# Performance work log

Hardware: AMD Instinct MI355X
Metric: run time of the kernel (lower is better)

Reference implementation:

```python
import jax, jax.numpy as jnp
import numpy as np

B, N, DN = 8, 4096, 64
E = 1048576
H, DM = 128, 64   # message MLP: 2*DN -> H -> DM
HU, F = 128, 64   # node-update MLP: DN+DM -> HU -> F


def setup_inputs() -> dict:
    key = jax.random.key(0)
    ks = jax.random.split(key, 13)
    inp = {
        'node_feats': jax.random.normal(ks[0], (B, N, DN), dtype=jnp.float32),
        'edge_b': jax.random.randint(ks[1], (E,), 0, B, dtype=jnp.int32),
        'edge_src': jax.random.randint(ks[2], (E,), 0, N, dtype=jnp.int32),
        'edge_dst': jax.random.randint(ks[3], (E,), 0, N, dtype=jnp.int32),
        'edge_vals': jax.random.uniform(ks[4], (E,), dtype=jnp.float32),
        # message MLP params (Dense-relu, Dense-linear)
        'Wm1': jax.random.normal(ks[5], (2 * DN, H), dtype=jnp.float32) / np.sqrt(2 * DN),
        'bm1': jnp.zeros((H,), jnp.float32),
        'Wm2': jax.random.normal(ks[6], (H, DM), dtype=jnp.float32) / np.sqrt(H),
        'bm2': jnp.zeros((DM,), jnp.float32),
        # node-update MLP params
        'Wu1': jax.random.normal(ks[7], (DN + DM, HU), dtype=jnp.float32) / np.sqrt(DN + DM),
        'bu1': jnp.zeros((HU,), jnp.float32),
        'Wu2': jax.random.normal(ks[8], (HU, F), dtype=jnp.float32) / np.sqrt(HU),
        'bu2': jnp.zeros((F,), jnp.float32),
    }
    return inp


def reference(node_feats, edge_b, edge_src, edge_dst, edge_vals,
              Wm1, bm1, Wm2, bm2, Wu1, bu1, Wu2, bu2):
    # --- create messages: gather src/target feats per edge ---
    src_feats = node_feats[edge_b, edge_src]            # (E, DN)
    tgt_feats = node_feats[edge_b, edge_dst]            # (E, DN)
    feats = jnp.concatenate([src_feats, tgt_feats], axis=-1)  # (E, 2*DN)
    h = jax.nn.relu(feats @ Wm1 + bm1)
    messages = h @ Wm2 + bm2                            # (E, DM)

    # --- gather (scatter) messages: weighted ragged segment-mean ---
    weighted = messages * edge_vals[:, None]            # (E, DM)
    seg = edge_b * N + edge_src                          # rowids b*max_N + src
    sums = jax.ops.segment_sum(weighted, seg, num_segments=B * N)
    counts = jax.ops.segment_sum(jnp.ones((E,), weighted.dtype), seg,
                                 num_segments=B * N)
    gathered = sums / jnp.maximum(counts, 1.0)[:, None]  # mean; 0 for empty rows
    gathered = gathered.reshape(B, N, DM)

    # --- update nodes ---
    upd_in = jnp.concatenate([node_feats, gathered], axis=-1)  # (B, N, DN+DM)
    hu = jax.nn.relu(upd_in @ Wu1 + bu1)
    updated = hu @ Wu2 + bu2                            # (B, N, F)
    return updated
```

## Files before the change

### kernel.cpp

```cpp
#include <hip/hip_runtime.h>

#define NB 8
#define NN 4096
#define DNF 64
#define NEDGE 1048576
#define DM 64
#define FF 64

#define NBKT2 2048
#define SPB2 16
#define NXCD 8
#define SUBCAP 176
#define OVFCAP 32768
#define SCATBLK 2048

using f32x4 = __attribute__((ext_vector_type(4))) float;
using f32x2 = __attribute__((ext_vector_type(2))) float;
using s16x8 = __attribute__((ext_vector_type(8))) short;

__device__ __forceinline__ unsigned short f2b(float f) {
    union { float f; unsigned u; } v; v.f = f;
    unsigned r = (v.u + 0x7fffu + ((v.u >> 16) & 1u)) >> 16;
    return (unsigned short)r;
}
__device__ __forceinline__ float uif(unsigned u) {
    union { unsigned u; float f; } v; v.u = u;
    return v.f;
}

__device__ __forceinline__ void pack_one(const float* __restrict__ W,
                                         unsigned short* __restrict__ out,
                                         int K, int Ncols, int idx) {
    int j = idx & 7;
    int lane = (idx >> 3) & 63;
    int frag = idx >> 9;
    int KS = K >> 5;
    int ks = frag % KS;
    int nt = frag / KS;
    int k = ks * 32 + ((lane >> 4) << 3) + j;
    int col = nt * 16 + (lane & 15);
    out[idx] = f2b(W[k * Ncols + col]);
}

__global__ void pack_all(const float* __restrict__ Wm1, const float* __restrict__ Wm2,
                         const float* __restrict__ Wu1, const float* __restrict__ Wu2,
                         unsigned short* __restrict__ Qw, unsigned short* __restrict__ Pw,
                         unsigned short* __restrict__ Wm2p,
                         unsigned short* __restrict__ Wu1p, unsigned short* __restrict__ Wu2p) {
    int idx = blockIdx.x * 256 + threadIdx.x;
    if (idx < 8192)        pack_one(Wm1,              Qw,   64, 128, idx);
    else if (idx < 16384)  pack_one(Wm1 + 64 * 128,   Pw,   64, 128, idx - 8192);
    else if (idx < 24576)  pack_one(Wm2,              Wm2p, 128, 64, idx - 16384);
    else if (idx < 40960)  pack_one(Wu1,              Wu1p, 128, 128, idx - 24576);
    else                   pack_one(Wu2,              Wu2p, 128, 64, idx - 40960);
}

__global__ void pack_weights(const float* __restrict__ W, unsigned short* __restrict__ out,
                             int K, int Ncols) {
    int idx = blockIdx.x * 256 + threadIdx.x;
    if (idx >= K * Ncols) return;
    pack_one(W, out, K, Ncols, idx);
}

__launch_bounds__(256, 6)
__global__ void scatter_pq(const int* __restrict__ eb, const int* __restrict__ esrc,
                           const int* __restrict__ edst, const float* __restrict__ evals,
                           unsigned* __restrict__ gcurP, unsigned* __restrict__ payslot,
                           unsigned* __restrict__ ovf_cnt, unsigned* __restrict__ ovf_seg,
                           unsigned* __restrict__ ovf_pay,
                           const float* __restrict__ X,
                           const unsigned short* __restrict__ Qw,
                           const unsigned short* __restrict__ Pw,
                           const float* __restrict__ b1,
                           unsigned short* __restrict__ Qp,
                           unsigned short* __restrict__ Pp) {
    __shared__ unsigned short A[64][72];
    if (blockIdx.x < SCATBLK) {
        unsigned xcd;
        asm volatile("s_getreg_b32 %0, hwreg(HW_REG_XCC_ID)" : "=s"(xcd));
        xcd &= (NXCD - 1);
        const int t0 = blockIdx.x * 512 + threadIdx.x;
        int seg[2]; unsigned pk[2];
#pragma unroll
        for (int k = 0; k < 2; ++k) {
            int e = t0 + k * 256;
            seg[k] = eb[e] * NN + esrc[e];
            unsigned wq = (unsigned)fminf(evals[e] * 8192.0f + 0.5f, 8191.0f);
            pk[k] = (unsigned)edst[e] | (wq << 12) | ((unsigned)(seg[k] & 15) << 25);
        }
        unsigned pos[2];
#pragma unroll
        for (int k = 0; k < 2; ++k)
            pos[k] = atomicAdd(&gcurP[((int)xcd * NBKT2 + (seg[k] >> 4)) * 16], 1u);
#pragma unroll
        for (int k = 0; k < 2; ++k) {
            if (pos[k] < (unsigned)SUBCAP) {
                payslot[((size_t)(seg[k] >> 4) * NXCD + xcd) * SUBCAP + pos[k]] = pk[k];
            } else {
                unsigned o = atomicAdd(ovf_cnt, 1u);
                if (o < (unsigned)OVFCAP) { ovf_seg[o] = (unsigned)seg[k]; ovf_pay[o] = pk[k]; }
            }
        }
    } else {
        const int tid = threadIdx.x;
        const int g0 = (blockIdx.x - SCATBLK) * 64;
        for (int i = 0; i < 16; ++i) {
            int idx = i * 256 + tid;
            int node = idx >> 6;
            int f = idx & 63;
            A[node][f] = f2b(X[(size_t)(g0 + node) * DNF + f]);
        }
        __syncthreads();
        const int wave = tid >> 6, lane = tid & 63;
        const int lr = lane & 15, lq = lane >> 4;
        const int arow = wave * 16 + lr;
        s16x8 a[2];
#pragma unroll
        for (int ks = 0; ks < 2; ++ks)
            a[ks] = *reinterpret_cast<const s16x8*>(&A[arow][ks * 32 + lq * 8]);
#pragma unroll
        for (int nt = 0; nt < 8; ++nt) {
            f32x4 accQ = {0.f, 0.f, 0.f, 0.f};
            f32x4 accP = {0.f, 0.f, 0.f, 0.f};
#pragma unroll
            for (int ks = 0; ks < 2; ++ks) {
                s16x8 bq = *reinterpret_cast<const s16x8*>(&Qw[(((nt << 1) + ks) * 64 + lane) * 8]);
                s16x8 bp = *reinterpret_cast<const s16x8*>(&Pw[(((nt << 1) + ks) * 64 + lane) * 8]);
                accQ = __builtin_amdgcn_mfma_f32_16x16x32_bf16(a[ks], bq, accQ, 0, 0, 0);
                accP = __builtin_amdgcn_mfma_f32_16x16x32_bf16(a[ks], bp, accP, 0, 0, 0);
            }
            int col = nt * 16 + lr;
            float bias = b1[col];
#pragma unroll
            for (int j = 0; j < 4; ++j) {
                int row = g0 + wave * 16 + lq * 4 + j;
                Qp[(size_t)row * 128 + col] = f2b(accQ[j] + bias);
                Pp[(size_t)row * 128 + col] = f2b(accP[j]);
            }
        }
    }
}

__launch_bounds__(256, 6)
__global__ void bucket16_fused(const unsigned short* __restrict__ Qp,
                               const unsigned short* __restrict__ Pp,
                               const unsigned* __restrict__ payslot,
                               const unsigned* __restrict__ gcurP,
                               const unsigned* __restrict__ ovf_cnt,
                               const unsigned* __restrict__ ovf_seg,
                               const unsigned* __restrict__ ovf_pay,
                               const unsigned short* __restrict__ Wm2p,
                               const float* __restrict__ b2m,
                               const float* __restrict__ X,
                               const unsigned short* __restrict__ Wu1p,
                               const float* __restrict__ bu1,
                               const unsigned short* __restrict__ Wu2p,
                               const float* __restrict__ bu2,
                               float* __restrict__ out) {
    __shared__ unsigned raw[NXCD * SUBCAP];
    __shared__ unsigned sorted[NXCD * SUBCAP];
    __shared__ unsigned short S[16][136];
    __shared__ unsigned short A1[16][136];
    __shared__ unsigned short Hs[16][136];
    __shared__ unsigned h4[4][16];
    __shared__ unsigned curb4[4][16];
    __shared__ unsigned offs[17];
    __shared__ unsigned cx[NXCD];
    __shared__ float SW[16], SC[16];
    const int tid = threadIdx.x, wv = tid >> 6, lane = tid & 63;
    const int bkt = (blockIdx.x & 7) * 256 + (blockIdx.x >> 3);
    const int node0 = bkt * SPB2;
    const int rowbase = (bkt >> 8) << 12;
    const unsigned novf = ovf_cnt[0];

#pragma unroll
    for (int i = 0; i < 4; ++i) {
        int idx = i * 256 + tid;
        int row = idx >> 6, f = idx & 63;
        A1[row][f] = f2b(X[(size_t)(node0 + row) * DNF + f]);
    }
    if (tid < 64) ((unsigned*)h4)[tid] = 0;
    if (tid < NXCD) cx[tid] = min(gcurP[(tid * NBKT2 + bkt) * 16], (unsigned)SUBCAP);
    __syncthreads();
#pragma unroll
    for (int xi = 0; xi < 2; ++xi) {
        int x = wv * 2 + xi;
        unsigned c = cx[x];
        for (unsigned i = lane; i < c; i += 64) {
            unsigned v = payslot[((size_t)bkt * NXCD + x) * SUBCAP + i];
            raw[x * SUBCAP + i] = v;
            atomicAdd(&h4[wv][(v >> 25) & 15u], 1u);
        }
    }
    __syncthreads();
    if (tid < 16) {
        int xx = (int)(h4[0][tid] + h4[1][tid] + h4[2][tid] + h4[3][tid]);
#pragma unroll
        for (int o = 1; o < 16; o <<= 1) {
            int y = __shfl_up(xx, o);
            if (tid >= o) xx += y;
        }
        offs[tid + 1] = (unsigned)xx;
        if (tid == 0) offs[0] = 0;
    }
    __syncthreads();
    if (tid < 64) {
        int w = tid >> 4, b = tid & 15;
        unsigned base = offs[b];
        for (int w2 = 0; w2 < w; ++w2) base += h4[w2][b];
        curb4[w][b] = base;
    }
    __syncthreads();
#pragma unroll
    for (int xi = 0; xi < 2; ++xi) {
        int x = wv * 2 + xi;
        unsigned c = cx[x];
        for (unsigned i = lane; i < c; i += 64) {
            unsigned v = raw[x * SUBCAP + i];
            unsigned pos = atomicAdd(&curb4[wv][(v >> 25) & 15u], 1u);
            sorted[pos] = v;
        }
    }
    __syncthreads();

    const unsigned* P32 = reinterpret_cast<const unsigned*>(Pp);
    const unsigned* Q32 = reinterpret_cast<const unsigned*>(Qp);
    const unsigned* PbS = P32 + (size_t)rowbase * 64;
    for (int si = 0; si < 4; ++si) {
        const int lo = wv * 4 + si;
        const int seg = node0 + lo;
        const unsigned s0 = offs[lo], s1 = offs[lo + 1];
        unsigned qv = Q32[(size_t)seg * 64 + lane];
        f32x2 q2 = { uif(qv << 16), uif(qv & 0xffff0000u) };
        f32x2 acc2 = { 0.f, 0.f };
        unsigned scnt = s1 - s0;

        float wl = 0.f;
        for (unsigned i = s0 + lane; i < s1; i += 64)
            wl += (float)((sorted[i] >> 12) & 8191u);
        for (int m2 = 1; m2 < 64; m2 <<= 1) wl += __shfl_xor(wl, m2);
        float wsum = wl;

        for (unsigned bse = s0; bse < s1; bse += 8) {
            unsigned pv[8]; float wf[8];
#pragma unroll
            for (int k = 0; k < 8; ++k) {
                unsigned idx = bse + (unsigned)k;
                unsigned cu = (idx < s1) ? sorted[idx] : 0u;
                int ci = __builtin_amdgcn_readfirstlane((int)cu);
                wf[k] = (float)(unsigned)((ci >> 12) & 8191);
                int row = ci & 0xfff;
                pv[k] = PbS[(size_t)row * 64 + lane];
            }
#pragma unroll
            for (int k = 0; k < 8; ++k) {
                f32x2 p2 = { uif(pv[k] << 16), uif(pv[k] & 0xffff0000u) };
                f32x2 h2 = q2 + p2;
                h2 = __builtin_elementwise_max(h2, (f32x2){0.f, 0.f});
                acc2 += wf[k] * h2;
            }
        }
        if (novf > 0) {
            unsigned ncl = min(novf, (unsigned)OVFCAP);
            for (unsigned i = 0; i < ncl; ++i) {
                if (ovf_seg[i] == (unsigned)seg) {
                    unsigned c = ovf_pay[i];
                    float w = (float)((c >> 12) & 8191u);
                    unsigned pv = PbS[(size_t)(c & 0xfffu) * 64 + lane];
                    f32x2 p2 = { uif(pv << 16), uif(pv & 0xffff0000u) };
                    f32x2 h2 = q2 + p2;
                    h2 = __builtin_elementwise_max(h2, (f32x2){0.f, 0.f});
                    acc2 += w * h2;
                    wsum += w;
                    scnt += 1;
                }
            }
        }
        unsigned sp = (unsigned)f2b(acc2.x) | ((unsigned)f2b(acc2.y) << 16);
        *reinterpret_cast<unsigned*>(&S[lo][2 * lane]) = sp;
        if (lane == 0) {
            SW[lo] = wsum;
            SC[lo] = (1.0f / 8192.0f) / (float)max(scnt, 1u);
        }
    }
    __syncthreads();

    const int lr = lane & 15, lq = lane >> 4;
    {
        s16x8 a[4];
#pragma unroll
        for (int ks = 0; ks < 4; ++ks)
            a[ks] = *reinterpret_cast<const s16x8*>(&S[lr][ks * 32 + lq * 8]);
        f32x4 acc = {0.f, 0.f, 0.f, 0.f};
#pragma unroll
        for (int ks = 0; ks < 4; ++ks) {
            s16x8 bf = *reinterpret_cast<const s16x8*>(&Wm2p[(((wv << 2) + ks) * 64 + lane) * 8]);
            acc = __builtin_amdgcn_mfma_f32_16x16x32_bf16(a[ks], bf, acc, 0, 0, 0);
        }
        float bb = b2m[wv * 16 + lr];
#pragma unroll
        for (int j = 0; j < 4; ++j) {
            int r = lq * 4 + j;
            float g = (acc[j] + SW[r] * bb) * SC[r];
            A1[r][64 + wv * 16 + lr] = f2b(g);
        }
    }
    __syncthreads();

    {
        s16x8 a1[4];
#pragma unroll
        for (int ks = 0; ks < 4; ++ks)
            a1[ks] = *reinterpret_cast<const s16x8*>(&A1[lr][ks * 32 + lq * 8]);
#pragma unroll
        for (int t = 0; t < 2; ++t) {
            int nt = wv * 2 + t;
            f32x4 acc = {0.f, 0.f, 0.f, 0.f};
#pragma unroll
            for (int ks = 0; ks < 4; ++ks) {
                s16x8 bf = *reinterpret_cast<const s16x8*>(&Wu1p[(((nt << 2) + ks) * 64 + lane) * 8]);
                acc = __builtin_amdgcn_mfma_f32_16x16x32_bf16(a1[ks], bf, acc, 0, 0, 0);
            }
            float bias = bu1[nt * 16 + lr];
#pragma unroll
            for (int j = 0; j < 4; ++j) {
                float hh = fmaxf(acc[j] + bias, 0.f);
                Hs[lq * 4 + j][nt * 16 + lr] = f2b(hh);
            }
        }
    }
    __syncthreads();

    {
        s16x8 a2[4];
#pragma unroll
        for (int ks = 0; ks < 4; ++ks)
            a2[ks] = *reinterpret_cast<const s16x8*>(&Hs[lr][ks * 32 + lq * 8]);
        f32x4 acc = {0.f, 0.f, 0.f, 0.f};
#pragma unroll
        for (int ks = 0; ks < 4; ++ks) {
            s16x8 bf = *reinterpret_cast<const s16x8*>(&Wu2p[(((wv << 2) + ks) * 64 + lane) * 8]);
            acc = __builtin_amdgcn_mfma_f32_16x16x32_bf16(a2[ks], bf, acc, 0, 0, 0);
        }
        float bias = bu2[wv * 16 + lr];
#pragma unroll
        for (int j = 0; j < 4; ++j)
            out[(size_t)(node0 + lq * 4 + j) * FF + wv * 16 + lr] = acc[j] + bias;
    }
}


template<int SCALE>
__launch_bounds__(256, 4)
__global__ void node_kernel(const float* __restrict__ node_feats,
                            const float* __restrict__ sums, const float* __restrict__ counts,
                            const unsigned short* __restrict__ W1p, const float* __restrict__ b1,
                            const unsigned short* __restrict__ W2p, const float* __restrict__ b2,
                            float* __restrict__ out) {
    __shared__ unsigned short A1[64][136];
    __shared__ unsigned short Hs[64][136];
    const int tid = threadIdx.x;
    const int g0 = blockIdx.x * 64;
    for (int i = 0; i < 16; ++i) {
        int idx = i * 256 + tid;
        int node = idx >> 6;
        int p = idx & 63;
        int g = g0 + node;
        float2 v;
        if (p < 32) {
            v = *reinterpret_cast<const float2*>(node_feats + (size_t)g * DNF + 2 * p);
        } else {
            float2 s = *reinterpret_cast<const float2*>(sums + (size_t)g * DM + 2 * p - 64);
            if (SCALE) {
                float scale = 1.0f / fmaxf(counts[g], 1.0f);
                s.x *= scale; s.y *= scale;
            }
            v = s;
        }
        unsigned packed = (unsigned)f2b(v.x) | ((unsigned)f2b(v.y) << 16);
        *reinterpret_cast<unsigned*>(&A1[node][2 * p]) = packed;
    }
    __syncthreads();
    const int wave = tid >> 6, lane = tid & 63;
    const int lr = lane & 15, lq = lane >> 4;
    const int arow = wave * 16 + lr;
    s16x8 a[4];
#pragma unroll
    for (int ks = 0; ks < 4; ++ks)
        a[ks] = *reinterpret_cast<const s16x8*>(&A1[arow][ks * 32 + lq * 8]);
#pragma unroll
    for (int nt = 0; nt < 8; ++nt) {
        f32x4 acc = {0.f, 0.f, 0.f, 0.f};
#pragma unroll
        for (int ks = 0; ks < 4; ++ks) {
            s16x8 bf = *reinterpret_cast<const s16x8*>(&W1p[(((nt << 2) + ks) * 64 + lane) * 8]);
            acc = __builtin_amdgcn_mfma_f32_16x16x32_bf16(a[ks], bf, acc, 0, 0, 0);
        }
        float bias = b1[nt * 16 + lr];
#pragma unroll
        for (int j = 0; j < 4; ++j) {
            float h = acc[j] + bias;
            h = h > 0.f ? h : 0.f;
            Hs[wave * 16 + lq * 4 + j][nt * 16 + lr] = f2b(h);
        }
    }
    s16x8 a2[4];
#pragma unroll
    for (int ks = 0; ks < 4; ++ks)
        a2[ks] = *reinterpret_cast<const s16x8*>(&Hs[arow][ks * 32 + lq * 8]);
#pragma unroll
    for (int nt = 0; nt < 4; ++nt) {
        f32x4 acc = {0.f, 0.f, 0.f, 0.f};
#pragma unroll
        for (int ks = 0; ks < 4; ++ks) {
            s16x8 bf = *reinterpret_cast<const s16x8*>(&W2p[(((nt << 2) + ks) * 64 + lane) * 8]);
            acc = __builtin_amdgcn_mfma_f32_16x16x32_bf16(a2[ks], bf, acc, 0, 0, 0);
        }
        float bias = b2[nt * 16 + lr];
#pragma unroll
        for (int j = 0; j < 4; ++j) {
            int g = g0 + wave * 16 + lq * 4 + j;
            out[(size_t)g * FF + nt * 16 + lr] = acc[j] + bias;
        }
    }
}

__launch_bounds__(256, 4)
__global__ void edge_kernel(const float* __restrict__ node_feats,
                            const int* __restrict__ eb, const int* __restrict__ esrc,
                            const int* __restrict__ edst, const float* __restrict__ evals,
                            const unsigned short* __restrict__ W1p, const float* __restrict__ b1,
                            const unsigned short* __restrict__ W2p, const float* __restrict__ b2,
                            float* __restrict__ sums, float* __restrict__ counts) {
    __shared__ unsigned short A1[64][136];
    __shared__ unsigned short Hs[64][136];
    const int tid = threadIdx.x;
    const int e0 = blockIdx.x * 64;
    if (tid < 64) {
        int e = e0 + tid;
        atomicAdd(&counts[eb[e] * NN + esrc[e]], 1.0f);
    }
    for (int i = 0; i < 16; ++i) {
        int idx = i * 256 + tid;
        int edge = idx >> 6;
        int p = idx & 63;
        int e = e0 + edge;
        int b = eb[e];
        const float* row;
        if (p < 32) row = node_feats + ((size_t)b * NN + esrc[e]) * DNF;
        else        row = node_feats + ((size_t)b * NN + edst[e]) * DNF - 64;
        float2 v = *reinterpret_cast<const float2*>(row + 2 * p);
        unsigned packed = (unsigned)f2b(v.x) | ((unsigned)f2b(v.y) << 16);
        *reinterpret_cast<unsigned*>(&A1[edge][2 * p]) = packed;
    }
    __syncthreads();
    const int wave = tid >> 6, lane = tid & 63;
    const int lr = lane & 15, lq = lane >> 4;
    const int arow = wave * 16 + lr;
    s16x8 a[4];
#pragma unroll
    for (int ks = 0; ks < 4; ++ks)
        a[ks] = *reinterpret_cast<const s16x8*>(&A1[arow][ks * 32 + lq * 8]);
#pragma unroll
    for (int nt = 0; nt < 8; ++nt) {
        f32x4 acc = {0.f, 0.f, 0.f, 0.f};
#pragma unroll
        for (int ks = 0; ks < 4; ++ks) {
            s16x8 bf = *reinterpret_cast<const s16x8*>(&W1p[(((nt << 2) + ks) * 64 + lane) * 8]);
            acc = __builtin_amdgcn_mfma_f32_16x16x32_bf16(a[ks], bf, acc, 0, 0, 0);
        }
        float bias = b1[nt * 16 + lr];
#pragma unroll
        for (int j = 0; j < 4; ++j) {
            float h = acc[j] + bias;
            h = h > 0.f ? h : 0.f;
            Hs[wave * 16 + lq * 4 + j][nt * 16 + lr] = f2b(h);
        }
    }
    s16x8 a2[4];
#pragma unroll
    for (int ks = 0; ks < 4; ++ks)
        a2[ks] = *reinterpret_cast<const s16x8*>(&Hs[arow][ks * 32 + lq * 8]);
    float ev[4]; int seg4[4];
#pragma unroll
    for (int j = 0; j < 4; ++j) {
        int r = e0 + wave * 16 + lq * 4 + j;
        ev[j] = evals[r];
        seg4[j] = eb[r] * NN + esrc[r];
    }
#pragma unroll
    for (int nt = 0; nt < 4; ++nt) {
        f32x4 acc = {0.f, 0.f, 0.f, 0.f};
#pragma unroll
        for (int ks = 0; ks < 4; ++ks) {
            s16x8 bf = *reinterpret_cast<const s16x8*>(&W2p[(((nt << 2) + ks) * 64 + lane) * 8]);
            acc = __builtin_amdgcn_mfma_f32_16x16x32_bf16(a2[ks], bf, acc, 0, 0, 0);
        }
        float bias = b2[nt * 16 + lr];
#pragma unroll
        for (int j = 0; j < 4; ++j) {
            float m = (acc[j] + bias) * ev[j];
            atomicAdd(&sums[(size_t)seg4[j] * DM + nt * 16 + lr], m);
        }
    }
}

extern "C" void kernel_launch(void* const* d_in, const int* in_sizes, int n_in,
                              void* d_out, int out_size, void* d_ws, size_t ws_size,
                              hipStream_t stream) {
    const float* node_feats = (const float*)d_in[0];
    const int*   eb    = (const int*)d_in[1];
    const int*   esrc  = (const int*)d_in[2];
    const int*   edst  = (const int*)d_in[3];
    const float* evals = (const float*)d_in[4];
    const float* Wm1 = (const float*)d_in[5];
    const float* bm1 = (const float*)d_in[6];
    const float* Wm2 = (const float*)d_in[7];
    const float* bm2 = (const float*)d_in[8];
    const float* Wu1 = (const float*)d_in[9];
    const float* bu1 = (const float*)d_in[10];
    const float* Wu2 = (const float*)d_in[11];
    const float* bu2 = (const float*)d_in[12];
    float* out = (float*)d_out;
    char* ws = (char*)d_ws;

    const size_t NEED = 29720704;
    if (ws_size >= NEED) {
        unsigned short* Qp      = (unsigned short*)(ws);
        unsigned short* Pp      = (unsigned short*)(ws + 8388608);
        unsigned*       payslot = (unsigned*)(ws + 16777216);
        unsigned*       gcurP   = (unsigned*)(ws + 28311552);
        unsigned*       ovf_cnt = (unsigned*)(ws + 29360128);
        unsigned*       ovf_seg = (unsigned*)(ws + 29360256);
        unsigned*       ovf_pay = (unsigned*)(ws + 29491328);
        unsigned short* Qw      = (unsigned short*)(ws + 29622400);
        unsigned short* Pw      = (unsigned short*)(ws + 29638784);
        unsigned short* Wu1p    = (unsigned short*)(ws + 29655168);
        unsigned short* Wu2p    = (unsigned short*)(ws + 29687936);
        unsigned short* Wm2p    = (unsigned short*)(ws + 29704320);

        hipMemsetAsync(gcurP, 0, 1048576 + 128, stream);
        pack_all<<<192, 256, 0, stream>>>(Wm1, Wm2, Wu1, Wu2, Qw, Pw, Wm2p, Wu1p, Wu2p);
        scatter_pq<<<SCATBLK + 512, 256, 0, stream>>>(eb, esrc, edst, evals,
                                                      gcurP, payslot, ovf_cnt, ovf_seg, ovf_pay,
                                                      node_feats, Qw, Pw, bm1, Qp, Pp);
        bucket16_fused<<<NBKT2, 256, 0, stream>>>(Qp, Pp, payslot, gcurP,
                                                  ovf_cnt, ovf_seg, ovf_pay,
                                                  Wm2p, bm2, node_feats,
                                                  Wu1p, bu1, Wu2p, bu2, out);
    } else {
        float* counts          = (float*)ws;
        unsigned short* W1p    = (unsigned short*)(ws + 131072);
        unsigned short* W2p    = (unsigned short*)(ws + 163840);
        unsigned short* Wu1p   = (unsigned short*)(ws + 180224);
        unsigned short* Wu2p   = (unsigned short*)(ws + 212992);
        hipMemsetAsync(d_out, 0, (size_t)out_size * sizeof(float), stream);
        hipMemsetAsync(counts, 0, 32768 * sizeof(float), stream);
        pack_weights<<<64, 256, 0, stream>>>(Wm1, W1p, 128, 128);
        pack_weights<<<32, 256, 0, stream>>>(Wm2, W2p, 128, 64);
        pack_weights<<<64, 256, 0, stream>>>(Wu1, Wu1p, 128, 128);
        pack_weights<<<32, 256, 0, stream>>>(Wu2, Wu2p, 128, 64);
        edge_kernel<<<NEDGE / 64, 256, 0, stream>>>(node_feats, eb, esrc, edst, evals,
                                                    W1p, bm1, W2p, bm2, out, counts);
        node_kernel<1><<<(NB * NN) / 64, 256, 0, stream>>>(node_feats, out, counts,
                                                           Wu1p, bu1, Wu2p, bu2, out);
    }
}
```

Baseline: 111.3 us.

## Replace atomic bucket scatter with histogram-scan counting sort of edges

Edges are now bucketed by a two-pass counting sort: per-block LDS histograms, a column-wise and total prefix scan, then a scatter using LDS atomic cursors into contiguous bucket ranges. The consumer kernel walks each bucket's exact range in chunks instead of fixed-capacity per-XCD slots plus an overflow list. This removes contended global atomics, the memset and the overflow scan. In exchange it adds extra kernel launches, a second read of edge indices, and a serial column scan with low parallelism.

After: 101.9 us. -8.4%, faster.

```diff
diff --git a/kernel.cpp b/kernel.cpp
--- a/kernel.cpp
+++ b/kernel.cpp
@@ -9,10 +9,9 @@
 
 #define NBKT2 2048
 #define SPB2 16
-#define NXCD 8
-#define SUBCAP 176
-#define OVFCAP 32768
-#define SCATBLK 2048
+#define SORTBLK 512
+#define EPB 2048
+#define CHUNK 1024
 
 using f32x4 = __attribute__((ext_vector_type(4))) float;
 using f32x2 = __attribute__((ext_vector_type(2))) float;
@@ -62,48 +61,33 @@
     pack_one(W, out, K, Ncols, idx);
 }
 
-__launch_bounds__(256, 6)
-__global__ void scatter_pq(const int* __restrict__ eb, const int* __restrict__ esrc,
-                           const int* __restrict__ edst, const float* __restrict__ evals,
-                           unsigned* __restrict__ gcurP, unsigned* __restrict__ payslot,
-                           unsigned* __restrict__ ovf_cnt, unsigned* __restrict__ ovf_seg,
-                           unsigned* __restrict__ ovf_pay,
-                           const float* __restrict__ X,
-                           const unsigned short* __restrict__ Qw,
-                           const unsigned short* __restrict__ Pw,
-                           const float* __restrict__ b1,
-                           unsigned short* __restrict__ Qp,
-                           unsigned short* __restrict__ Pp) {
-    __shared__ unsigned short A[64][72];
-    if (blockIdx.x < SCATBLK) {
-        unsigned xcd;
-        asm volatile("s_getreg_b32 %0, hwreg(HW_REG_XCC_ID)" : "=s"(xcd));
-        xcd &= (NXCD - 1);
-        const int t0 = blockIdx.x * 512 + threadIdx.x;
-        int seg[2]; unsigned pk[2];
-#pragma unroll
-        for (int k = 0; k < 2; ++k) {
-            int e = t0 + k * 256;
-            seg[k] = eb[e] * NN + esrc[e];
-            unsigned wq = (unsigned)fminf(evals[e] * 8192.0f + 0.5f, 8191.0f);
-            pk[k] = (unsigned)edst[e] | (wq << 12) | ((unsigned)(seg[k] & 15) << 25);
-        }
-        unsigned pos[2];
-#pragma unroll
-        for (int k = 0; k < 2; ++k)
-            pos[k] = atomicAdd(&gcurP[((int)xcd * NBKT2 + (seg[k] >> 4)) * 16], 1u);
-#pragma unroll
-        for (int k = 0; k < 2; ++k) {
-            if (pos[k] < (unsigned)SUBCAP) {
-                payslot[((size_t)(seg[k] >> 4) * NXCD + xcd) * SUBCAP + pos[k]] = pk[k];
-            } else {
-                unsigned o = atomicAdd(ovf_cnt, 1u);
-                if (o < (unsigned)OVFCAP) { ovf_seg[o] = (unsigned)seg[k]; ovf_pay[o] = pk[k]; }
-            }
-        }
+__launch_bounds__(256, 8)
+__global__ void hist_pq(const int* __restrict__ eb, const int* __restrict__ esrc,
+                        unsigned* __restrict__ histm,
+                        const float* __restrict__ X,
+                        const unsigned short* __restrict__ Qw,
+                        const unsigned short* __restrict__ Pw,
+                        const float* __restrict__ b1,
+                        unsigned short* __restrict__ Qp,
+                        unsigned short* __restrict__ Pp) {
+    __shared__ unsigned lds_u[2304];
+    const int tid = threadIdx.x;
+    if (blockIdx.x < SORTBLK) {
+        unsigned* bins = lds_u;
+        for (int i = tid; i < NBKT2; i += 256) bins[i] = 0;
+        __syncthreads();
+        const int e0 = blockIdx.x * EPB;
+#pragma unroll
+        for (int i = 0; i < EPB / 256; ++i) {
+            int e = e0 + i * 256 + tid;
+            atomicAdd(&bins[(eb[e] * NN + esrc[e]) >> 4], 1u);
+        }
+        __syncthreads();
+        for (int i = tid; i < NBKT2; i += 256)
+            histm[(size_t)blockIdx.x * NBKT2 + i] = bins[i];
     } else {
-        const int tid = threadIdx.x;
-        const int g0 = (blockIdx.x - SCATBLK) * 64;
+        unsigned short (*A)[72] = reinterpret_cast<unsigned short(*)[72]>(lds_u);
+        const int g0 = (blockIdx.x - SORTBLK) * 64;
         for (int i = 0; i < 16; ++i) {
             int idx = i * 256 + tid;
             int node = idx >> 6;
@@ -141,14 +125,67 @@
     }
 }
 
+__launch_bounds__(256)
+__global__ void scan_cols(unsigned* __restrict__ histm, unsigned* __restrict__ total) {
+    const int col = blockIdx.x * 256 + threadIdx.x;
+    unsigned run = 0;
+    for (int b = 0; b < SORTBLK; ++b) {
+        unsigned v = histm[(size_t)b * NBKT2 + col];
+        histm[(size_t)b * NBKT2 + col] = run;
+        run += v;
+    }
+    total[col] = run;
+}
+
+__launch_bounds__(256)
+__global__ void scan_tot(const unsigned* __restrict__ total, unsigned* __restrict__ base) {
+    __shared__ unsigned part[256];
+    const int t = threadIdx.x;
+    unsigned v[8]; unsigned s = 0;
+#pragma unroll
+    for (int i = 0; i < 8; ++i) { v[i] = total[t * 8 + i]; s += v[i]; }
+    part[t] = s;
+    __syncthreads();
+    for (int off = 1; off < 256; off <<= 1) {
+        unsigned x = (t >= off) ? part[t - off] : 0u;
+        __syncthreads();
+        part[t] += x;
+        __syncthreads();
+    }
+    unsigned run = t ? part[t - 1] : 0u;
+#pragma unroll
+    for (int i = 0; i < 8; ++i) { base[t * 8 + i] = run; run += v[i]; }
+    if (t == 255) base[NBKT2] = run;
+}
+
+__launch_bounds__(256, 8)
+__global__ void sort_scatter(const int* __restrict__ eb, const int* __restrict__ esrc,
+                             const int* __restrict__ edst, const float* __restrict__ evals,
+                             const unsigned* __restrict__ histm,
+                             const unsigned* __restrict__ base,
+                             unsigned* __restrict__ payslot) {
+    __shared__ unsigned cur[NBKT2];
+    const int blk = blockIdx.x, tid = threadIdx.x;
+    for (int i = tid; i < NBKT2; i += 256)
+        cur[i] = base[i] + histm[(size_t)blk * NBKT2 + i];
+    __syncthreads();
+    const int e0 = blk * EPB;
+#pragma unroll
+    for (int i = 0; i < EPB / 256; ++i) {
+        int e = e0 + i * 256 + tid;
+        int seg = eb[e] * NN + esrc[e];
+        unsigned wq = (unsigned)fminf(evals[e] * 8192.0f + 0.5f, 8191.0f);
+        unsigned pay = (unsigned)edst[e] | (wq << 12) | ((unsigned)(seg & 15) << 25);
+        unsigned pos = atomicAdd(&cur[seg >> 4], 1u);
+        payslot[pos] = pay;
+    }
+}
+
 __launch_bounds__(256, 6)
 __global__ void bucket16_fused(const unsigned short* __restrict__ Qp,
                                const unsigned short* __restrict__ Pp,
                                const unsigned* __restrict__ payslot,
-                               const unsigned* __restrict__ gcurP,
-                               const unsigned* __restrict__ ovf_cnt,
-                               const unsigned* __restrict__ ovf_seg,
-                               const unsigned* __restrict__ ovf_pay,
+                               const unsigned* __restrict__ gBase,
                                const unsigned short* __restrict__ Wm2p,
                                const float* __restrict__ b2m,
                                const float* __restrict__ X,
@@ -157,21 +194,19 @@
                                const unsigned short* __restrict__ Wu2p,
                                const float* __restrict__ bu2,
                                float* __restrict__ out) {
-    __shared__ unsigned raw[NXCD * SUBCAP];
-    __shared__ unsigned sorted[NXCD * SUBCAP];
+    __shared__ unsigned raw[CHUNK];
+    __shared__ unsigned sorted[CHUNK];
     __shared__ unsigned short S[16][136];
     __shared__ unsigned short A1[16][136];
     __shared__ unsigned short Hs[16][136];
     __shared__ unsigned h4[4][16];
     __shared__ unsigned curb4[4][16];
     __shared__ unsigned offs[17];
-    __shared__ unsigned cx[NXCD];
     __shared__ float SW[16], SC[16];
     const int tid = threadIdx.x, wv = tid >> 6, lane = tid & 63;
     const int bkt = (blockIdx.x & 7) * 256 + (blockIdx.x >> 3);
     const int node0 = bkt * SPB2;
     const int rowbase = (bkt >> 8) << 12;
-    const unsigned novf = ovf_cnt[0];
 
 #pragma unroll
     for (int i = 0; i < 4; ++i) {
@@ -179,108 +214,101 @@
         int row = idx >> 6, f = idx & 63;
         A1[row][f] = f2b(X[(size_t)(node0 + row) * DNF + f]);
     }
-    if (tid < 64) ((unsigned*)h4)[tid] = 0;
-    if (tid < NXCD) cx[tid] = min(gcurP[(tid * NBKT2 + bkt) * 16], (unsigned)SUBCAP);
-    __syncthreads();
-#pragma unroll
-    for (int xi = 0; xi < 2; ++xi) {
-        int x = wv * 2 + xi;
-        unsigned c = cx[x];
-        for (unsigned i = lane; i < c; i += 64) {
-            unsigned v = payslot[((size_t)bkt * NXCD + x) * SUBCAP + i];
-            raw[x * SUBCAP + i] = v;
-            atomicAdd(&h4[wv][(v >> 25) & 15u], 1u);
-        }
-    }
-    __syncthreads();
-    if (tid < 16) {
-        int xx = (int)(h4[0][tid] + h4[1][tid] + h4[2][tid] + h4[3][tid]);
-#pragma unroll
-        for (int o = 1; o < 16; o <<= 1) {
-            int y = __shfl_up(xx, o);
-            if (tid >= o) xx += y;
-        }
-        offs[tid + 1] = (unsigned)xx;
-        if (tid == 0) offs[0] = 0;
-    }
-    __syncthreads();
-    if (tid < 64) {
-        int w = tid >> 4, b = tid & 15;
-        unsigned base = offs[b];
-        for (int w2 = 0; w2 < w; ++w2) base += h4[w2][b];
-        curb4[w][b] = base;
-    }
-    __syncthreads();
-#pragma unroll
-    for (int xi = 0; xi < 2; ++xi) {
-        int x = wv * 2 + xi;
-        unsigned c = cx[x];
-        for (unsigned i = lane; i < c; i += 64) {
-            unsigned v = raw[x * SUBCAP + i];
-            unsigned pos = atomicAdd(&curb4[wv][(v >> 25) & 15u], 1u);
-            sorted[pos] = v;
-        }
-    }
-    __syncthreads();
 
     const unsigned* P32 = reinterpret_cast<const unsigned*>(Pp);
     const unsigned* Q32 = reinterpret_cast<const unsigned*>(Qp);
     const unsigned* PbS = P32 + (size_t)rowbase * 64;
+
+    f32x2 q2[4], acc2[4];
+    float wsum[4];
+    unsigned scnt[4];
+#pragma unroll
+    for (int si = 0; si < 4; ++si) {
+        int lo = wv * 4 + si;
+        unsigned qv = Q32[(size_t)(node0 + lo) * 64 + lane];
+        q2[si].x = uif(qv << 16); q2[si].y = uif(qv & 0xffff0000u);
+        acc2[si].x = 0.f; acc2[si].y = 0.f;
+        wsum[si] = 0.f; scnt[si] = 0u;
+    }
+
+    const unsigned start = gBase[bkt], end = gBase[bkt + 1];
+    for (unsigned cbase = start; cbase < end; cbase += CHUNK) {
+        const unsigned n = min((unsigned)CHUNK, end - cbase);
+        if (tid < 64) ((unsigned*)h4)[tid] = 0;
+        __syncthreads();
+        for (unsigned i = tid; i < n; i += 256) {
+            unsigned v = payslot[cbase + i];
+            raw[i] = v;
+            atomicAdd(&h4[wv][(v >> 25) & 15u], 1u);
+        }
+        __syncthreads();
+        if (tid < 16) {
+            int xx = (int)(h4[0][tid] + h4[1][tid] + h4[2][tid] + h4[3][tid]);
+#pragma unroll
+            for (int o = 1; o < 16; o <<= 1) {
+                int y = __shfl_up(xx, o);
+                if (tid >= o) xx += y;
+            }
+            offs[tid + 1] = (unsigned)xx;
+            if (tid == 0) offs[0] = 0;
+        }
+        __syncthreads();
+        if (tid < 64) {
+            int w = tid >> 4, b = tid & 15;
+            unsigned bse = offs[b];
+            for (int w2 = 0; w2 < w; ++w2) bse += h4[w2][b];
+            curb4[w][b] = bse;
+        }
+        __syncthreads();
+        for (unsigned i = tid; i < n; i += 256) {
+            unsigned v = raw[i];
+            unsigned pos = atomicAdd(&curb4[wv][(v >> 25) & 15u], 1u);
+            sorted[pos] = v;
+        }
+        __syncthreads();
+
+#pragma unroll
+        for (int si = 0; si < 4; ++si) {
+            const int lo = wv * 4 + si;
+            const unsigned s0 = offs[lo], s1 = offs[lo + 1];
+            scnt[si] += s1 - s0;
+            float wl = 0.f;
+            for (unsigned i = s0 + lane; i < s1; i += 64)
+                wl += (float)((sorted[i] >> 12) & 8191u);
+            for (int m2 = 1; m2 < 64; m2 <<= 1) wl += __shfl_xor(wl, m2);
+            wsum[si] += wl;
+
+            for (unsigned bse = s0; bse < s1; bse += 8) {
+                unsigned pv[8]; float wf[8];
+#pragma unroll
+                for (int k = 0; k < 8; ++k) {
+                    unsigned idx = bse + (unsigned)k;
+                    unsigned cu = (idx < s1) ? sorted[idx] : 0u;
+                    int ci = __builtin_amdgcn_readfirstlane((int)cu);
+                    wf[k] = (float)(unsigned)((ci >> 12) & 8191);
+                    int row = ci & 0xfff;
+                    pv[k] = PbS[(size_t)row * 64 + lane];
+                }
+#pragma unroll
+                for (int k = 0; k < 8; ++k) {
+                    f32x2 p2 = { uif(pv[k] << 16), uif(pv[k] & 0xffff0000u) };
+                    f32x2 h2 = q2[si] + p2;
+                    h2 = __builtin_elementwise_max(h2, (f32x2){0.f, 0.f});
+                    acc2[si] += wf[k] * h2;
+                }
+            }
+        }
+        __syncthreads();
+    }
+
+#pragma unroll
     for (int si = 0; si < 4; ++si) {
         const int lo = wv * 4 + si;
-        const int seg = node0 + lo;
-        const unsigned s0 = offs[lo], s1 = offs[lo + 1];
-        unsigned qv = Q32[(size_t)seg * 64 + lane];
-        f32x2 q2 = { uif(qv << 16), uif(qv & 0xffff0000u) };
-        f32x2 acc2 = { 0.f, 0.f };
-        unsigned scnt = s1 - s0;
-
-        float wl = 0.f;
-        for (unsigned i = s0 + lane; i < s1; i += 64)
-            wl += (float)((sorted[i] >> 12) & 8191u);
-        for (int m2 = 1; m2 < 64; m2 <<= 1) wl += __shfl_xor(wl, m2);
-        float wsum = wl;
-
-        for (unsigned bse = s0; bse < s1; bse += 8) {
-            unsigned pv[8]; float wf[8];
-#pragma unroll
-            for (int k = 0; k < 8; ++k) {
-                unsigned idx = bse + (unsigned)k;
-                unsigned cu = (idx < s1) ? sorted[idx] : 0u;
-                int ci = __builtin_amdgcn_readfirstlane((int)cu);
-                wf[k] = (float)(unsigned)((ci >> 12) & 8191);
-                int row = ci & 0xfff;
-                pv[k] = PbS[(size_t)row * 64 + lane];
-            }
-#pragma unroll
-            for (int k = 0; k < 8; ++k) {
-                f32x2 p2 = { uif(pv[k] << 16), uif(pv[k] & 0xffff0000u) };
-                f32x2 h2 = q2 + p2;
-                h2 = __builtin_elementwise_max(h2, (f32x2){0.f, 0.f});
-                acc2 += wf[k] * h2;
-            }
-        }
-        if (novf > 0) {
-            unsigned ncl = min(novf, (unsigned)OVFCAP);
-            for (unsigned i = 0; i < ncl; ++i) {
-                if (ovf_seg[i] == (unsigned)seg) {
-                    unsigned c = ovf_pay[i];
-                    float w = (float)((c >> 12) & 8191u);
-                    unsigned pv = PbS[(size_t)(c & 0xfffu) * 64 + lane];
-                    f32x2 p2 = { uif(pv << 16), uif(pv & 0xffff0000u) };
-                    f32x2 h2 = q2 + p2;
-                    h2 = __builtin_elementwise_max(h2, (f32x2){0.f, 0.f});
-                    acc2 += w * h2;
-                    wsum += w;
-                    scnt += 1;
-                }
-            }
-        }
-        unsigned sp = (unsigned)f2b(acc2.x) | ((unsigned)f2b(acc2.y) << 16);
+        unsigned sp = (unsigned)f2b(acc2[si].x) | ((unsigned)f2b(acc2[si].y) << 16);
         *reinterpret_cast<unsigned*>(&S[lo][2 * lane]) = sp;
         if (lane == 0) {
-            SW[lo] = wsum;
-            SC[lo] = (1.0f / 8192.0f) / (float)max(scnt, 1u);
+            SW[lo] = wsum[si];
+            SC[lo] = (1.0f / 8192.0f) / (float)max(scnt[si], 1u);
         }
     }
     __syncthreads();
@@ -524,28 +552,28 @@
     float* out = (float*)d_out;
     char* ws = (char*)d_ws;
 
-    const size_t NEED = 29720704;
+    const size_t NEED = 25296896;
     if (ws_size >= NEED) {
         unsigned short* Qp      = (unsigned short*)(ws);
         unsigned short* Pp      = (unsigned short*)(ws + 8388608);
         unsigned*       payslot = (unsigned*)(ws + 16777216);
-        unsigned*       gcurP   = (unsigned*)(ws + 28311552);
-        unsigned*       ovf_cnt = (unsigned*)(ws + 29360128);
-        unsigned*       ovf_seg = (unsigned*)(ws + 29360256);
-        unsigned*       ovf_pay = (unsigned*)(ws + 29491328);
-        unsigned short* Qw      = (unsigned short*)(ws + 29622400);
-        unsigned short* Pw      = (unsigned short*)(ws + 29638784);
-        unsigned short* Wu1p    = (unsigned short*)(ws + 29655168);
-        unsigned short* Wu2p    = (unsigned short*)(ws + 29687936);
-        unsigned short* Wm2p    = (unsigned short*)(ws + 29704320);
-
-        hipMemsetAsync(gcurP, 0, 1048576 + 128, stream);
+        unsigned*       histm   = (unsigned*)(ws + 20971520);
+        unsigned*       total   = (unsigned*)(ws + 25165824);
+        unsigned*       bbase   = (unsigned*)(ws + 25182208);
+        unsigned short* Qw      = (unsigned short*)(ws + 25198592);
+        unsigned short* Pw      = (unsigned short*)(ws + 25214976);
+        unsigned short* Wu1p    = (unsigned short*)(ws + 25231360);
+        unsigned short* Wu2p    = (unsigned short*)(ws + 25264128);
+        unsigned short* Wm2p    = (unsigned short*)(ws + 25280512);
+
         pack_all<<<192, 256, 0, stream>>>(Wm1, Wm2, Wu1, Wu2, Qw, Pw, Wm2p, Wu1p, Wu2p);
-        scatter_pq<<<SCATBLK + 512, 256, 0, stream>>>(eb, esrc, edst, evals,
-                                                      gcurP, payslot, ovf_cnt, ovf_seg, ovf_pay,
-                                                      node_feats, Qw, Pw, bm1, Qp, Pp);
-        bucket16_fused<<<NBKT2, 256, 0, stream>>>(Qp, Pp, payslot, gcurP,
-                                                  ovf_cnt, ovf_seg, ovf_pay,
+        hist_pq<<<SORTBLK + 512, 256, 0, stream>>>(eb, esrc, histm,
+                                                   node_feats, Qw, Pw, bm1, Qp, Pp);
+        scan_cols<<<NBKT2 / 256, 256, 0, stream>>>(histm, total);
+        scan_tot<<<1, 256, 0, stream>>>(total, bbase);
+        sort_scatter<<<SORTBLK, 256, 0, stream>>>(eb, esrc, edst, evals,
+                                                  histm, bbase, payslot);
+        bucket16_fused<<<NBKT2, 256, 0, stream>>>(Qp, Pp, payslot, bbase,
                                                   Wm2p, bm2, node_feats,
                                                   Wu1p, bu1, Wu2p, bu2, out);
     } else {
```

## Replace atomic bucket scatter with block-histogram counting sort of edges by segment

Applied to the files above, without the earlier changes.

Replaces the per-XCD atomic bucketing with overflow lists with a deterministic counting sort. A per-block LDS histogram using packed 16-bit counters is followed by a column scan, a total scan, and a scatter that places each edge directly at its segment's global position. The Q projection moves into the fused bucket kernel, computed from LDS, which drops the Qp global buffer and the in-block sort and overflow scan. The cost is three extra kernel launches and a 16 MB histogram matrix that is written, scanned column-serially and read back.

After: 116.0 us (median of 5 runs). 4.2% more time.

```diff
diff --git a/kernel.cpp b/kernel.cpp
--- a/kernel.cpp
+++ b/kernel.cpp
@@ -7,12 +7,10 @@
 #define DM 64
 #define FF 64
 
-#define NBKT2 2048
 #define SPB2 16
-#define NXCD 8
-#define SUBCAP 176
-#define OVFCAP 32768
-#define SCATBLK 2048
+#define NSEG 32768
+#define SORTBLK2 256
+#define EPB2 4096
 
 using f32x4 = __attribute__((ext_vector_type(4))) float;
 using f32x2 = __attribute__((ext_vector_type(2))) float;
@@ -62,52 +60,33 @@
     pack_one(W, out, K, Ncols, idx);
 }
 
-__launch_bounds__(256, 6)
-__global__ void scatter_pq(const int* __restrict__ eb, const int* __restrict__ esrc,
-                           const int* __restrict__ edst, const float* __restrict__ evals,
-                           unsigned* __restrict__ gcurP, unsigned* __restrict__ payslot,
-                           unsigned* __restrict__ ovf_cnt, unsigned* __restrict__ ovf_seg,
-                           unsigned* __restrict__ ovf_pay,
-                           const float* __restrict__ X,
-                           const unsigned short* __restrict__ Qw,
-                           const unsigned short* __restrict__ Pw,
-                           const float* __restrict__ b1,
-                           unsigned short* __restrict__ Qp,
-                           unsigned short* __restrict__ Pp) {
-    __shared__ unsigned short A[64][72];
-    if (blockIdx.x < SCATBLK) {
-        unsigned xcd;
-        asm volatile("s_getreg_b32 %0, hwreg(HW_REG_XCC_ID)" : "=s"(xcd));
-        xcd &= (NXCD - 1);
-        const int t0 = blockIdx.x * 512 + threadIdx.x;
-        int seg[2]; unsigned pk[2];
-#pragma unroll
-        for (int k = 0; k < 2; ++k) {
-            int e = t0 + k * 256;
-            seg[k] = eb[e] * NN + esrc[e];
-            unsigned wq = (unsigned)fminf(evals[e] * 8192.0f + 0.5f, 8191.0f);
-            pk[k] = (unsigned)edst[e] | (wq << 12) | ((unsigned)(seg[k] & 15) << 25);
-        }
-        unsigned pos[2];
-#pragma unroll
-        for (int k = 0; k < 2; ++k)
-            pos[k] = atomicAdd(&gcurP[((int)xcd * NBKT2 + (seg[k] >> 4)) * 16], 1u);
-#pragma unroll
-        for (int k = 0; k < 2; ++k) {
-            if (pos[k] < (unsigned)SUBCAP) {
-                payslot[((size_t)(seg[k] >> 4) * NXCD + xcd) * SUBCAP + pos[k]] = pk[k];
-            } else {
-                unsigned o = atomicAdd(ovf_cnt, 1u);
-                if (o < (unsigned)OVFCAP) { ovf_seg[o] = (unsigned)seg[k]; ovf_pay[o] = pk[k]; }
-            }
-        }
+__launch_bounds__(512, 4)
+__global__ void hist_p(const int* __restrict__ eb, const int* __restrict__ esrc,
+                       unsigned short* __restrict__ histm16,
+                       const float* __restrict__ X,
+                       const unsigned short* __restrict__ Pw,
+                       unsigned short* __restrict__ Pp) {
+    __shared__ unsigned lds_u[16384];
+    const int tid = threadIdx.x;
+    if (blockIdx.x < SORTBLK2) {
+        for (int i = tid; i < 16384; i += 512) lds_u[i] = 0;
+        __syncthreads();
+        const int e0 = blockIdx.x * EPB2;
+#pragma unroll
+        for (int i = 0; i < EPB2 / 512; ++i) {
+            int e = e0 + i * 512 + tid;
+            int seg = eb[e] * NN + esrc[e];
+            atomicAdd(&lds_u[seg >> 1], 1u << ((seg & 1) * 16));
+        }
+        __syncthreads();
+        unsigned* out32 = reinterpret_cast<unsigned*>(histm16) + (size_t)blockIdx.x * 16384;
+        for (int i = tid; i < 16384; i += 512) out32[i] = lds_u[i];
     } else {
-        const int tid = threadIdx.x;
-        const int g0 = (blockIdx.x - SCATBLK) * 64;
+        unsigned short (*A)[72] = reinterpret_cast<unsigned short(*)[72]>(lds_u);
+        const int g0 = (blockIdx.x - SORTBLK2) * 128;
         for (int i = 0; i < 16; ++i) {
-            int idx = i * 256 + tid;
-            int node = idx >> 6;
-            int f = idx & 63;
+            int idx = i * 512 + tid;
+            int node = idx >> 6, f = idx & 63;
             A[node][f] = f2b(X[(size_t)(g0 + node) * DNF + f]);
         }
         __syncthreads();
@@ -120,35 +99,86 @@
             a[ks] = *reinterpret_cast<const s16x8*>(&A[arow][ks * 32 + lq * 8]);
 #pragma unroll
         for (int nt = 0; nt < 8; ++nt) {
-            f32x4 accQ = {0.f, 0.f, 0.f, 0.f};
             f32x4 accP = {0.f, 0.f, 0.f, 0.f};
 #pragma unroll
             for (int ks = 0; ks < 2; ++ks) {
-                s16x8 bq = *reinterpret_cast<const s16x8*>(&Qw[(((nt << 1) + ks) * 64 + lane) * 8]);
                 s16x8 bp = *reinterpret_cast<const s16x8*>(&Pw[(((nt << 1) + ks) * 64 + lane) * 8]);
-                accQ = __builtin_amdgcn_mfma_f32_16x16x32_bf16(a[ks], bq, accQ, 0, 0, 0);
                 accP = __builtin_amdgcn_mfma_f32_16x16x32_bf16(a[ks], bp, accP, 0, 0, 0);
             }
             int col = nt * 16 + lr;
-            float bias = b1[col];
 #pragma unroll
             for (int j = 0; j < 4; ++j) {
                 int row = g0 + wave * 16 + lq * 4 + j;
-                Qp[(size_t)row * 128 + col] = f2b(accQ[j] + bias);
                 Pp[(size_t)row * 128 + col] = f2b(accP[j]);
             }
         }
     }
 }
 
-__launch_bounds__(256, 6)
-__global__ void bucket16_fused(const unsigned short* __restrict__ Qp,
-                               const unsigned short* __restrict__ Pp,
+__launch_bounds__(256)
+__global__ void scan_cols(unsigned short* __restrict__ histm16, unsigned* __restrict__ totals) {
+    const int col = blockIdx.x * 256 + threadIdx.x;
+    unsigned run = 0;
+    for (int b = 0; b < SORTBLK2; ++b) {
+        unsigned v = histm16[(size_t)b * NSEG + col];
+        histm16[(size_t)b * NSEG + col] = (unsigned short)run;
+        run += v;
+    }
+    totals[col] = run;
+}
+
+__launch_bounds__(1024)
+__global__ void scan_tot(const unsigned* __restrict__ totals, unsigned* __restrict__ segBase) {
+    __shared__ unsigned part[1024];
+    const int t = threadIdx.x;
+    unsigned v[32]; unsigned s = 0;
+#pragma unroll
+    for (int i = 0; i < 32; ++i) { v[i] = totals[t * 32 + i]; s += v[i]; }
+    part[t] = s;
+    __syncthreads();
+    for (int off = 1; off < 1024; off <<= 1) {
+        unsigned x = (t >= off) ? part[t - off] : 0u;
+        __syncthreads();
+        part[t] += x;
+        __syncthreads();
+    }
+    unsigned run = t ? part[t - 1] : 0u;
+#pragma unroll
+    for (int i = 0; i < 32; ++i) { segBase[t * 32 + i] = run; run += v[i]; }
+    if (t == 1023) segBase[NSEG] = run;
+}
+
+__launch_bounds__(512, 4)
+__global__ void sort_scatter(const int* __restrict__ eb, const int* __restrict__ esrc,
+                             const int* __restrict__ edst, const float* __restrict__ evals,
+                             const unsigned short* __restrict__ histm16,
+                             const unsigned* __restrict__ segBase,
+                             unsigned* __restrict__ payslot) {
+    __shared__ unsigned curP[16384];
+    const int tid = threadIdx.x, blk = blockIdx.x;
+    for (int i = tid; i < 16384; i += 512) curP[i] = 0;
+    __syncthreads();
+    const unsigned short* hrow = histm16 + (size_t)blk * NSEG;
+    const int e0 = blk * EPB2;
+#pragma unroll
+    for (int i = 0; i < EPB2 / 512; ++i) {
+        int e = e0 + i * 512 + tid;
+        int seg = eb[e] * NN + esrc[e];
+        unsigned wq = (unsigned)fminf(evals[e] * 8192.0f + 0.5f, 8191.0f);
+        unsigned pay = (unsigned)edst[e] | (wq << 12);
+        unsigned sh = (unsigned)(seg & 1) * 16u;
+        unsigned old = atomicAdd(&curP[seg >> 1], 1u << sh);
+        unsigned l = (old >> sh) & 0xffffu;
+        payslot[segBase[seg] + (unsigned)hrow[seg] + l] = pay;
+    }
+}
+
+__launch_bounds__(256, 8)
+__global__ void bucket16_fused(const unsigned short* __restrict__ Pp,
                                const unsigned* __restrict__ payslot,
-                               const unsigned* __restrict__ gcurP,
-                               const unsigned* __restrict__ ovf_cnt,
-                               const unsigned* __restrict__ ovf_seg,
-                               const unsigned* __restrict__ ovf_pay,
+                               const unsigned* __restrict__ segBase,
+                               const unsigned short* __restrict__ Qw,
+                               const float* __restrict__ b1,
                                const unsigned short* __restrict__ Wm2p,
                                const float* __restrict__ b2m,
                                const float* __restrict__ X,
@@ -157,21 +187,16 @@
                                const unsigned short* __restrict__ Wu2p,
                                const float* __restrict__ bu2,
                                float* __restrict__ out) {
-    __shared__ unsigned raw[NXCD * SUBCAP];
-    __shared__ unsigned sorted[NXCD * SUBCAP];
+    __shared__ unsigned short A1[16][136];
+    __shared__ unsigned short Qs[16][136];
     __shared__ unsigned short S[16][136];
-    __shared__ unsigned short A1[16][136];
     __shared__ unsigned short Hs[16][136];
-    __shared__ unsigned h4[4][16];
-    __shared__ unsigned curb4[4][16];
-    __shared__ unsigned offs[17];
-    __shared__ unsigned cx[NXCD];
     __shared__ float SW[16], SC[16];
     const int tid = threadIdx.x, wv = tid >> 6, lane = tid & 63;
     const int bkt = (blockIdx.x & 7) * 256 + (blockIdx.x >> 3);
     const int node0 = bkt * SPB2;
     const int rowbase = (bkt >> 8) << 12;
-    const unsigned novf = ovf_cnt[0];
+    const int lr = lane & 15, lq = lane >> 4;
 
 #pragma unroll
     for (int i = 0; i < 4; ++i) {
@@ -179,74 +204,48 @@
         int row = idx >> 6, f = idx & 63;
         A1[row][f] = f2b(X[(size_t)(node0 + row) * DNF + f]);
     }
-    if (tid < 64) ((unsigned*)h4)[tid] = 0;
-    if (tid < NXCD) cx[tid] = min(gcurP[(tid * NBKT2 + bkt) * 16], (unsigned)SUBCAP);
-    __syncthreads();
-#pragma unroll
-    for (int xi = 0; xi < 2; ++xi) {
-        int x = wv * 2 + xi;
-        unsigned c = cx[x];
-        for (unsigned i = lane; i < c; i += 64) {
-            unsigned v = payslot[((size_t)bkt * NXCD + x) * SUBCAP + i];
-            raw[x * SUBCAP + i] = v;
-            atomicAdd(&h4[wv][(v >> 25) & 15u], 1u);
-        }
-    }
-    __syncthreads();
-    if (tid < 16) {
-        int xx = (int)(h4[0][tid] + h4[1][tid] + h4[2][tid] + h4[3][tid]);
-#pragma unroll
-        for (int o = 1; o < 16; o <<= 1) {
-            int y = __shfl_up(xx, o);
-            if (tid >= o) xx += y;
-        }
-        offs[tid + 1] = (unsigned)xx;
-        if (tid == 0) offs[0] = 0;
-    }
-    __syncthreads();
-    if (tid < 64) {
-        int w = tid >> 4, b = tid & 15;
-        unsigned base = offs[b];
-        for (int w2 = 0; w2 < w; ++w2) base += h4[w2][b];
-        curb4[w][b] = base;
-    }
-    __syncthreads();
-#pragma unroll
-    for (int xi = 0; xi < 2; ++xi) {
-        int x = wv * 2 + xi;
-        unsigned c = cx[x];
-        for (unsigned i = lane; i < c; i += 64) {
-            unsigned v = raw[x * SUBCAP + i];
-            unsigned pos = atomicAdd(&curb4[wv][(v >> 25) & 15u], 1u);
-            sorted[pos] = v;
+    __syncthreads();
+
+    {
+        s16x8 a[2];
+#pragma unroll
+        for (int ks = 0; ks < 2; ++ks)
+            a[ks] = *reinterpret_cast<const s16x8*>(&A1[lr][ks * 32 + lq * 8]);
+#pragma unroll
+        for (int t = 0; t < 2; ++t) {
+            int nt = wv * 2 + t;
+            f32x4 acc = {0.f, 0.f, 0.f, 0.f};
+#pragma unroll
+            for (int ks = 0; ks < 2; ++ks) {
+                s16x8 bq = *reinterpret_cast<const s16x8*>(&Qw[(((nt << 1) + ks) * 64 + lane) * 8]);
+                acc = __builtin_amdgcn_mfma_f32_16x16x32_bf16(a[ks], bq, acc, 0, 0, 0);
+            }
+            int col = nt * 16 + lr;
+            float bias = b1[col];
+#pragma unroll
+            for (int j = 0; j < 4; ++j)
+                Qs[lq * 4 + j][col] = f2b(acc[j] + bias);
         }
     }
     __syncthreads();
 
     const unsigned* P32 = reinterpret_cast<const unsigned*>(Pp);
-    const unsigned* Q32 = reinterpret_cast<const unsigned*>(Qp);
     const unsigned* PbS = P32 + (size_t)rowbase * 64;
     for (int si = 0; si < 4; ++si) {
         const int lo = wv * 4 + si;
         const int seg = node0 + lo;
-        const unsigned s0 = offs[lo], s1 = offs[lo + 1];
-        unsigned qv = Q32[(size_t)seg * 64 + lane];
+        const unsigned s0 = segBase[seg], s1 = segBase[seg + 1];
+        unsigned qv = *reinterpret_cast<const unsigned*>(&Qs[lo][2 * lane]);
         f32x2 q2 = { uif(qv << 16), uif(qv & 0xffff0000u) };
         f32x2 acc2 = { 0.f, 0.f };
-        unsigned scnt = s1 - s0;
-
-        float wl = 0.f;
-        for (unsigned i = s0 + lane; i < s1; i += 64)
-            wl += (float)((sorted[i] >> 12) & 8191u);
-        for (int m2 = 1; m2 < 64; m2 <<= 1) wl += __shfl_xor(wl, m2);
-        float wsum = wl;
+        float wsum = 0.f;
 
         for (unsigned bse = s0; bse < s1; bse += 8) {
             unsigned pv[8]; float wf[8];
 #pragma unroll
             for (int k = 0; k < 8; ++k) {
                 unsigned idx = bse + (unsigned)k;
-                unsigned cu = (idx < s1) ? sorted[idx] : 0u;
+                unsigned cu = (idx < s1) ? payslot[idx] : 0u;
                 int ci = __builtin_amdgcn_readfirstlane((int)cu);
                 wf[k] = (float)(unsigned)((ci >> 12) & 8191);
                 int row = ci & 0xfff;
@@ -258,34 +257,18 @@
                 f32x2 h2 = q2 + p2;
                 h2 = __builtin_elementwise_max(h2, (f32x2){0.f, 0.f});
                 acc2 += wf[k] * h2;
-            }
-        }
-        if (novf > 0) {
-            unsigned ncl = min(novf, (unsigned)OVFCAP);
-            for (unsigned i = 0; i < ncl; ++i) {
-                if (ovf_seg[i] == (unsigned)seg) {
-                    unsigned c = ovf_pay[i];
-                    float w = (float)((c >> 12) & 8191u);
-                    unsigned pv = PbS[(size_t)(c & 0xfffu) * 64 + lane];
-                    f32x2 p2 = { uif(pv << 16), uif(pv & 0xffff0000u) };
-                    f32x2 h2 = q2 + p2;
-                    h2 = __builtin_elementwise_max(h2, (f32x2){0.f, 0.f});
-                    acc2 += w * h2;
-                    wsum += w;
-                    scnt += 1;
-                }
+                wsum += wf[k];
             }
         }
         unsigned sp = (unsigned)f2b(acc2.x) | ((unsigned)f2b(acc2.y) << 16);
         *reinterpret_cast<unsigned*>(&S[lo][2 * lane]) = sp;
         if (lane == 0) {
             SW[lo] = wsum;
-            SC[lo] = (1.0f / 8192.0f) / (float)max(scnt, 1u);
-        }
-    }
-    __syncthreads();
-
-    const int lr = lane & 15, lq = lane >> 4;
+            SC[lo] = (1.0f / 8192.0f) / (float)max(s1 - s0, 1u);
+        }
+    }
+    __syncthreads();
+
     {
         s16x8 a[4];
 #pragma unroll
@@ -526,28 +509,26 @@
 
     const size_t NEED = 29720704;
     if (ws_size >= NEED) {
-        unsigned short* Qp      = (unsigned short*)(ws);
-        unsigned short* Pp      = (unsigned short*)(ws + 8388608);
-        unsigned*       payslot = (unsigned*)(ws + 16777216);
-        unsigned*       gcurP   = (unsigned*)(ws + 28311552);
-        unsigned*       ovf_cnt = (unsigned*)(ws + 29360128);
-        unsigned*       ovf_seg = (unsigned*)(ws + 29360256);
-        unsigned*       ovf_pay = (unsigned*)(ws + 29491328);
+        unsigned short* Pp      = (unsigned short*)(ws);
+        unsigned*       payslot = (unsigned*)(ws + 8388608);
+        unsigned short* histm16 = (unsigned short*)(ws + 12582912);
+        unsigned*       segBase = (unsigned*)(ws + 29360128);
+        unsigned*       totals  = (unsigned*)(ws + 29491328);
         unsigned short* Qw      = (unsigned short*)(ws + 29622400);
         unsigned short* Pw      = (unsigned short*)(ws + 29638784);
         unsigned short* Wu1p    = (unsigned short*)(ws + 29655168);
         unsigned short* Wu2p    = (unsigned short*)(ws + 29687936);
         unsigned short* Wm2p    = (unsigned short*)(ws + 29704320);
 
-        hipMemsetAsync(gcurP, 0, 1048576 + 128, stream);
         pack_all<<<192, 256, 0, stream>>>(Wm1, Wm2, Wu1, Wu2, Qw, Pw, Wm2p, Wu1p, Wu2p);
-        scatter_pq<<<SCATBLK + 512, 256, 0, stream>>>(eb, esrc, edst, evals,
-                                                      gcurP, payslot, ovf_cnt, ovf_seg, ovf_pay,
-                                                      node_feats, Qw, Pw, bm1, Qp, Pp);
-        bucket16_fused<<<NBKT2, 256, 0, stream>>>(Qp, Pp, payslot, gcurP,
-                                                  ovf_cnt, ovf_seg, ovf_pay,
-                                                  Wm2p, bm2, node_feats,
-                                                  Wu1p, bu1, Wu2p, bu2, out);
+        hist_p<<<2 * SORTBLK2, 512, 0, stream>>>(eb, esrc, histm16, node_feats, Pw, Pp);
+        scan_cols<<<NSEG / 256, 256, 0, stream>>>(histm16, totals);
+        scan_tot<<<1, 1024, 0, stream>>>(totals, segBase);
+        sort_scatter<<<SORTBLK2, 512, 0, stream>>>(eb, esrc, edst, evals,
+                                                   histm16, segBase, payslot);
+        bucket16_fused<<<NSEG / SPB2, 256, 0, stream>>>(Pp, payslot, segBase,
+                                                        Qw, bm1, Wm2p, bm2, node_feats,
+                                                        Wu1p, bu1, Wu2p, bu2, out);
     } else {
         float* counts          = (float*)ws;
         unsigned short* W1p    = (unsigned short*)(ws + 131072);
```
